# Optimization experiments

Measured on AMD Instinct MI355X. Metric: run time of the kernel, lower is better.

Reference implementation:

```python
import jax, jax.numpy as jnp
import numpy as np

FRS = np.array([1, 2, 4, 8, 16, 25, 36, 50, 75], dtype=np.float32)
N_EXPERTS = len(FRS)
N = 1048576
DIMS = [(4, 32), (32, 32), (32, 64), (64, 64)]


def setup_inputs() -> dict:
    key = jax.random.key(0)
    ks = jax.random.split(key, 2 + 8)
    # features: col 0 = framerate drawn from the known framerate set, cols 1:5 = affinity feats
    fr_idx = jax.random.randint(ks[0], (N,), 0, N_EXPERTS)
    framerates = jnp.asarray(FRS)[fr_idx]
    aff = jax.random.normal(ks[1], (N, 4), dtype=jnp.float32)
    features = jnp.concatenate([framerates[:, None], aff], axis=1)
    # stacked per-expert MLP params (torch Linear: y = x @ W.T + b; store W as [in,out])
    params = {}
    scale = 0.1
    for li, (din, dout) in enumerate(DIMS):
        params[f"W{li+1}"] = scale * jax.random.normal(ks[2 + 2 * li], (N_EXPERTS, din, dout), dtype=jnp.float32)
        params[f"b{li+1}"] = scale * jax.random.normal(ks[3 + 2 * li], (N_EXPERTS, dout), dtype=jnp.float32)
    return {"features": features, **params}


def _expert_mlp(x, W1, b1, W2, b2, W3, b3, W4, b4):
    h = jax.nn.relu(x @ W1 + b1)
    h = jax.nn.relu(h @ W2 + b2)
    h = jax.nn.relu(h @ W3 + b3)
    return h @ W4 + b4  # [N, 64]


def reference(features, W1, b1, W2, b2, W3, b3, W4, b4):
    frs = jnp.asarray(FRS)
    framerates = features[:, 0]
    x = features[:, 1:]  # [N, 4] (ignore_appr=False)
    # nearest-framerate expert index (argmin picks first min, matching find_index)
    k = jnp.argmin(jnp.abs(framerates[:, None] - frs[None, :]), axis=1)  # [N]
    pred = jnp.zeros(features.shape[0], dtype=features.dtype)
    for e in range(N_EXPERTS):  # fixed, small expert set
        out_e = _expert_mlp(x, W1[e], b1[e], W2[e], b2[e], W3[e], b3[e], W4[e], b4[e])
        pred = jnp.where(k == e, out_e.sum(axis=1), pred)
    return pred
```

## Files before the change

kernel.cpp:

```cpp
#include <hip/hip_runtime.h>
#include <stdint.h>

#define NEXP 9
#define FTHR 512
#define RPH 4
#define SBLK (FTHR * RPH)
#define PADSLK (SBLK + NEXP * 32)
#define MAXT 80
#define TBL_BYTES 7936
#define CLS_STRIDE 168

typedef float f32x4 __attribute__((ext_vector_type(4)));
typedef float f32x16 __attribute__((ext_vector_type(16)));
typedef _Float16 f16x8 __attribute__((ext_vector_type(8)));

struct alignas(16) I4 { int a, b, c, d; };
struct alignas(64) Q4 { f32x4 a, b, c, d; };

__device__ __forceinline__ int pk(float a, float b) {
    return __builtin_bit_cast(int, __builtin_amdgcn_cvt_pkrtz(a, b));
}
__device__ __forceinline__ f32x16 zero16() {
    f32x16 z;
#pragma unroll
    for (int r = 0; r < 16; ++r) z[r] = 0.f;
    return z;
}

__device__ __forceinline__ int expert_of(float fr) {
    const float frs[NEXP] = {1.f, 2.f, 4.f, 8.f, 16.f, 25.f, 36.f, 50.f, 75.f};
    int k = 0;
    float best = fabsf(fr - frs[0]);
#pragma unroll
    for (int e = 1; e < NEXP; ++e) {
        float d = fabsf(fr - frs[e]);
        if (d < best) { best = d; k = e; }
    }
    return k;
}

__global__ __launch_bounds__(256) void k_prep(const float* __restrict__ W1, const float* __restrict__ b1,
                                              const float* __restrict__ W2, const float* __restrict__ b2,
                                              const float* __restrict__ W3, const float* __restrict__ b3,
                                              const float* __restrict__ W4, const float* __restrict__ b4,
                                              char* __restrict__ tab) {
    int e = blockIdx.x;
    int tid = threadIdx.x;
    char* T = tab + (size_t)e * TBL_BYTES;

    __shared__ float psum[64][4];
    __shared__ float rs2[64];
    __shared__ float b4s_s;
    {
        int row = tid >> 2, q = tid & 3;
        const float* w = W4 + (size_t)e * 4096 + row * 64 + q * 16;
        f32x4 a = *(const f32x4*)(w + 0), b = *(const f32x4*)(w + 4);
        f32x4 c = *(const f32x4*)(w + 8), d = *(const f32x4*)(w + 12);
        psum[row][q] = (a.x + a.y + a.z + a.w) + (b.x + b.y + b.z + b.w)
                     + (c.x + c.y + c.z + c.w) + (d.x + d.y + d.z + d.w);
    }
    __syncthreads();
    if (tid < 64) {
        int l = tid, g = l >> 5, m = l & 31;
        rs2[l] = psum[l][0] + psum[l][1] + psum[l][2] + psum[l][3];
        float bp = b4[e * 64 + l];
#pragma unroll
        for (int d = 1; d < 64; d <<= 1) bp += __shfl_xor(bp, d, 64);
        if (l == 0) b4s_s = bp;

        {
            f16x8 v;
#pragma unroll
            for (int ei = 0; ei < 8; ++ei) {
                int k = g * 8 + ei;
                float w = (k < 4) ? W1[e * 128 + k * 32 + m] : (k == 4 ? b1[e * 32 + m] : 0.f);
                v[ei] = (_Float16)w;
            }
            *(f16x8*)(T + 0 * 1024 + l * 16) = v;
        }
#pragma unroll
        for (int kf = 0; kf < 2; ++kf) {
            f16x8 v;
#pragma unroll
            for (int ei = 0; ei < 8; ++ei) {
                int row = kf * 16 + (ei & 3) + 8 * (ei >> 2) + 4 * g;
                v[ei] = (_Float16)W2[e * 1024 + row * 32 + m];
            }
            *(f16x8*)(T + (1 + kf) * 1024 + l * 16) = v;
        }
#pragma unroll
        for (int t = 0; t < 2; ++t)
#pragma unroll
            for (int kf = 0; kf < 2; ++kf) {
                f16x8 v;
#pragma unroll
                for (int ei = 0; ei < 8; ++ei) {
                    int row = kf * 16 + (ei & 3) + 8 * (ei >> 2) + 4 * g;
                    v[ei] = (_Float16)W3[e * 2048 + row * 64 + t * 32 + m];
                }
                *(f16x8*)(T + (3 + t * 2 + kf) * 1024 + l * 16) = v;
            }
    }
    __syncthreads();
    if (tid < 32) {
        int g = tid >> 4, r = tid & 15;
        int row = (r & 3) + 8 * (r >> 2) + 4 * g;
        float* C = (float*)(T + 7168);
        C[0 * 32 + tid] = b2[e * 32 + row];
        C[1 * 32 + tid] = b3[e * 64 + row];
        C[2 * 32 + tid] = b3[e * 64 + 32 + row];
        C[3 * 32 + tid] = rs2[row];
        C[4 * 32 + tid] = rs2[32 + row];
        if (tid == 0) C[160] = b4s_s;
    }
}

__global__ __launch_bounds__(FTHR, 4) void k_main(const float* __restrict__ feat, int n,
                                                  const char* __restrict__ tab,
                                                  float* __restrict__ out) {
    __shared__ uint2 bx[PADSLK];
    __shared__ unsigned short bidx[PADSLK];
    __shared__ float cls[NEXP * CLS_STRIDE];
    __shared__ int lcnt[NEXP];
    __shared__ int pbase[NEXP];
    __shared__ int wbase[RPH][8][NEXP];
    __shared__ unsigned char tile_e[MAXT];
    __shared__ short tile_s[MAXT];
    __shared__ unsigned char tile_v[MAXT];
    __shared__ int nt_s;

    int bid = blockIdx.x, tid = threadIdx.x;
    int wid = tid >> 6, lane = tid & 63, g = lane >> 5, m = lane & 31;
    int gbase = bid * SBLK;

    if (tid < NEXP) lcnt[tid] = 0;
    {
        uint2 z = {0u, 0u};
#pragma unroll
        for (int q = 0; q < 5; ++q) {
            int o = q * FTHR + tid;
            if (o < PADSLK) bx[o] = z;
        }
    }
    {
        const float* tf = (const float*)tab;
        for (int idx = tid; idx < NEXP * 161; idx += FTHR) {
            int e = idx / 161, o = idx - e * 161;
            cls[e * CLS_STRIDE + o] = tf[e * (TBL_BYTES / 4) + 1792 + o];
        }
    }
    __syncthreads();

    int kk[RPH], rk[RPH];
    uint2 xw[RPH];
#pragma unroll
    for (int r = 0; r < RPH; ++r) {
        int i = gbase + r * FTHR + tid;
        int k = -1;
        uint2 w = {0u, 0u};
        if (i < n) {
            const float* f = feat + (size_t)i * 5;
            k = expert_of(f[0]);
            w.x = (unsigned)pk(f[1], f[2]);
            w.y = (unsigned)pk(f[3], f[4]);
        }
        kk[r] = k; xw[r] = w;
        unsigned long long myM = 0;
#pragma unroll
        for (int e = 0; e < NEXP; ++e) {
            unsigned long long mm = __ballot(k == e);
            if (k == e) myM = mm;
            if (lane == 0) {
                int c = __popcll(mm);
                wbase[r][wid][e] = c ? atomicAdd(&lcnt[e], c) : 0;
            }
        }
        rk[r] = __popcll(myM & ((1ull << lane) - 1ull));
    }
    __syncthreads();

    if (wid == 0) {
        int e = lane;
        int c = (e < NEXP) ? lcnt[e] : 0;
        int ntl = (c + 31) >> 5;
        int padc = ntl << 5;
        int sp = padc, st = ntl;
#pragma unroll
        for (int d = 1; d < 16; d <<= 1) {
            int a = __shfl_up(sp, d, 64);
            int b = __shfl_up(st, d, 64);
            if (lane >= d) { sp += a; st += b; }
        }
        if (e < NEXP) {
            int pb = sp - padc, tb = st - ntl;
            pbase[e] = pb;
            for (int j = 0; j < ntl; ++j) {
                tile_e[tb + j] = (unsigned char)e;
                tile_s[tb + j] = (short)(pb + j * 32);
                int v = c - j * 32;
                tile_v[tb + j] = (unsigned char)(v > 32 ? 32 : v);
            }
            if (e == NEXP - 1) nt_s = st;
        }
    }
    __syncthreads();

#pragma unroll
    for (int r = 0; r < RPH; ++r) {
        int k = kk[r];
        if (k >= 0) {
            int slot = pbase[k] + wbase[r][wid][k] + rk[r];
            bx[slot] = xw[r];
            bidx[slot] = (unsigned short)(r * FTHR + tid);
        }
    }
    __syncthreads();

    int nt = nt_s;
    int t0 = (wid * nt) >> 3, t1 = ((wid + 1) * nt) >> 3;
    int cur_e = -1;
    f16x8 A1 = {}, A2a = {}, A2b = {}, A30a = {}, A30b = {}, A31a = {}, A31b = {};
    f32x16 W40r = zero16(), W41r = zero16();
    float b4v = 0.f;
    const float* Cc = cls;
    for (int t = t0; t < t1; ++t) {
        int e = __builtin_amdgcn_readfirstlane((int)tile_e[t]);
        if (e != cur_e) {
            cur_e = e;
            const char* T = tab + (size_t)e * TBL_BYTES;
            A1 = *(const f16x8*)(T + 0 * 1024 + lane * 16);
            A2a = *(const f16x8*)(T + 1 * 1024 + lane * 16);
            A2b = *(const f16x8*)(T + 2 * 1024 + lane * 16);
            A30a = *(const f16x8*)(T + 3 * 1024 + lane * 16);
            A30b = *(const f16x8*)(T + 4 * 1024 + lane * 16);
            A31a = *(const f16x8*)(T + 5 * 1024 + lane * 16);
            A31b = *(const f16x8*)(T + 6 * 1024 + lane * 16);
            Cc = cls + e * CLS_STRIDE + g * 16;
            {
                Q4 q;
                const float* c = Cc + 3 * 32;
                q.a = *(const f32x4*)(c + 0); q.b = *(const f32x4*)(c + 4);
                q.c = *(const f32x4*)(c + 8); q.d = *(const f32x4*)(c + 12);
                W40r = __builtin_bit_cast(f32x16, q);
                const float* c2 = Cc + 4 * 32;
                q.a = *(const f32x4*)(c2 + 0); q.b = *(const f32x4*)(c2 + 4);
                q.c = *(const f32x4*)(c2 + 8); q.d = *(const f32x4*)(c2 + 12);
                W41r = __builtin_bit_cast(f32x16, q);
            }
            b4v = cls[e * CLS_STRIDE + 160];
        }
        auto ldC = [&](int mat) -> f32x16 {
            const float* c = Cc + mat * 32;
            Q4 q;
            q.a = *(const f32x4*)(c + 0);
            q.b = *(const f32x4*)(c + 4);
            q.c = *(const f32x4*)(c + 8);
            q.d = *(const f32x4*)(c + 12);
            return __builtin_bit_cast(f32x16, q);
        };

        int s = tile_s[t], v = tile_v[t];
        uint2 xv = bx[s + m];

        I4 b1i = {g ? 0 : (int)xv.x, g ? 0 : (int)xv.y, g ? 0 : 0x3C00, 0};
        f16x8 B1 = __builtin_bit_cast(f16x8, b1i);

        f32x16 d1 = __builtin_amdgcn_mfma_f32_32x32x16_f16(A1, B1, zero16(), 0, 0, 0);
#pragma unroll
        for (int r = 0; r < 16; ++r) d1[r] = fmaxf(d1[r], 0.f);
        I4 p0 = {pk(d1[0], d1[1]), pk(d1[2], d1[3]), pk(d1[4], d1[5]), pk(d1[6], d1[7])};
        I4 p1 = {pk(d1[8], d1[9]), pk(d1[10], d1[11]), pk(d1[12], d1[13]), pk(d1[14], d1[15])};
        f16x8 B2a = __builtin_bit_cast(f16x8, p0);
        f16x8 B2b = __builtin_bit_cast(f16x8, p1);

        f32x16 d2 = __builtin_amdgcn_mfma_f32_32x32x16_f16(A2a, B2a, ldC(0), 0, 0, 0);
        d2 = __builtin_amdgcn_mfma_f32_32x32x16_f16(A2b, B2b, d2, 0, 0, 0);
#pragma unroll
        for (int r = 0; r < 16; ++r) d2[r] = fmaxf(d2[r], 0.f);
        I4 q0 = {pk(d2[0], d2[1]), pk(d2[2], d2[3]), pk(d2[4], d2[5]), pk(d2[6], d2[7])};
        I4 q1 = {pk(d2[8], d2[9]), pk(d2[10], d2[11]), pk(d2[12], d2[13]), pk(d2[14], d2[15])};
        f16x8 B3a = __builtin_bit_cast(f16x8, q0);
        f16x8 B3b = __builtin_bit_cast(f16x8, q1);

        float acc = 0.f;
        {
            f32x16 d3 = __builtin_amdgcn_mfma_f32_32x32x16_f16(A30a, B3a, ldC(1), 0, 0, 0);
            d3 = __builtin_amdgcn_mfma_f32_32x32x16_f16(A30b, B3b, d3, 0, 0, 0);
#pragma unroll
            for (int r = 0; r < 16; ++r) acc += fmaxf(d3[r], 0.f) * W40r[r];
        }
        {
            f32x16 d3 = __builtin_amdgcn_mfma_f32_32x32x16_f16(A31a, B3a, ldC(2), 0, 0, 0);
            d3 = __builtin_amdgcn_mfma_f32_32x32x16_f16(A31b, B3b, d3, 0, 0, 0);
#pragma unroll
            for (int r = 0; r < 16; ++r) acc += fmaxf(d3[r], 0.f) * W41r[r];
        }
        acc += __shfl_xor(acc, 32, 64);
        float rres = acc + b4v;
        if (!g && m < v) out[gbase + (int)bidx[s + m]] = rres;
    }
}

__global__ __launch_bounds__(256) void k_fallback(const float* __restrict__ feat,
                                                  const float* __restrict__ W1, const float* __restrict__ b1,
                                                  const float* __restrict__ W2, const float* __restrict__ b2,
                                                  const float* __restrict__ W3, const float* __restrict__ b3,
                                                  const float* __restrict__ W4, const float* __restrict__ b4,
                                                  float* __restrict__ out, int n) {
    int i = blockIdx.x * 256 + threadIdx.x;
    if (i >= n) return;
    const float* f = feat + (size_t)i * 5;
    int e = expert_of(f[0]);
    float x0 = f[1], x1 = f[2], x2 = f[3], x3 = f[4];
    float h1[32], h2[32], h3[64];
    for (int j = 0; j < 32; ++j) {
        float a = b1[e * 32 + j];
        a += x0 * W1[e * 128 + 0 * 32 + j];
        a += x1 * W1[e * 128 + 1 * 32 + j];
        a += x2 * W1[e * 128 + 2 * 32 + j];
        a += x3 * W1[e * 128 + 3 * 32 + j];
        h1[j] = fmaxf(a, 0.f);
    }
    for (int j = 0; j < 32; ++j) h2[j] = b2[e * 32 + j];
    for (int i2 = 0; i2 < 32; ++i2)
        for (int j = 0; j < 32; ++j) h2[j] += h1[i2] * W2[e * 1024 + i2 * 32 + j];
    for (int j = 0; j < 32; ++j) h2[j] = fmaxf(h2[j], 0.f);
    for (int j = 0; j < 64; ++j) h3[j] = b3[e * 64 + j];
    for (int i2 = 0; i2 < 32; ++i2)
        for (int j = 0; j < 64; ++j) h3[j] += h2[i2] * W3[e * 2048 + i2 * 64 + j];
    float pred = 0.f;
    for (int o = 0; o < 64; ++o) pred += b4[e * 64 + o];
    for (int j = 0; j < 64; ++j) {
        float rsum = 0.f;
        for (int o = 0; o < 64; ++o) rsum += W4[e * 4096 + j * 64 + o];
        pred += fmaxf(h3[j], 0.f) * rsum;
    }
    out[i] = pred;
}

extern "C" void kernel_launch(void* const* d_in, const int* in_sizes, int n_in,
                              void* d_out, int out_size, void* d_ws, size_t ws_size,
                              hipStream_t stream) {
    const float* feat = (const float*)d_in[0];
    const float* W1 = (const float*)d_in[1];
    const float* b1 = (const float*)d_in[2];
    const float* W2 = (const float*)d_in[3];
    const float* b2 = (const float*)d_in[4];
    const float* W3 = (const float*)d_in[5];
    const float* b3 = (const float*)d_in[6];
    const float* W4 = (const float*)d_in[7];
    const float* b4 = (const float*)d_in[8];
    float* out = (float*)d_out;
    int n = in_sizes[0] / 5;

    const size_t need = (size_t)NEXP * TBL_BYTES;

    if (ws_size >= need) {
        char* tab = (char*)d_ws;
        k_prep<<<NEXP, 256, 0, stream>>>(W1, b1, W2, b2, W3, b3, W4, b4, tab);
        int nb = (n + SBLK - 1) / SBLK;
        k_main<<<nb, FTHR, 0, stream>>>(feat, n, tab, out);
    } else {
        k_fallback<<<(n + 255) / 256, 256, 0, stream>>>(feat, W1, b1, W2, b2, W3, b3, W4, b4, out, n);
    }
}
```

Measured before the change: 33.55 us.

## Move final layer reduction to MFMA, use packed f16 ReLU, halve rows per block

```diff
diff --git a/kernel.cpp b/kernel.cpp
--- a/kernel.cpp
+++ b/kernel.cpp
@@ -3,12 +3,12 @@
 
 #define NEXP 9
 #define FTHR 512
-#define RPH 4
+#define RPH 2
 #define SBLK (FTHR * RPH)
 #define PADSLK (SBLK + NEXP * 32)
-#define MAXT 80
+#define MAXT 48
 #define TBL_BYTES 7936
-#define CLS_STRIDE 168
+#define CLS_STRIDE 136
 
 typedef float f32x4 __attribute__((ext_vector_type(4)));
 typedef float f32x16 __attribute__((ext_vector_type(16)));
@@ -20,6 +20,13 @@
 __device__ __forceinline__ int pk(float a, float b) {
     return __builtin_bit_cast(int, __builtin_amdgcn_cvt_pkrtz(a, b));
 }
+__device__ __forceinline__ int pkh(float a, float b) {
+    int p = pk(a, b);
+    int r;
+    int z = 0;
+    asm("v_pk_max_f16 %0, %1, %2" : "=v"(r) : "v"(p), "v"(z));
+    return r;
+}
 __device__ __forceinline__ f32x16 zero16() {
     f32x16 z;
 #pragma unroll
@@ -28,15 +35,8 @@
 }
 
 __device__ __forceinline__ int expert_of(float fr) {
-    const float frs[NEXP] = {1.f, 2.f, 4.f, 8.f, 16.f, 25.f, 36.f, 50.f, 75.f};
-    int k = 0;
-    float best = fabsf(fr - frs[0]);
-#pragma unroll
-    for (int e = 1; e < NEXP; ++e) {
-        float d = fabsf(fr - frs[e]);
-        if (d < best) { best = d; k = e; }
-    }
-    return k;
+    return (fr > 1.5f) + (fr > 3.f) + (fr > 6.f) + (fr > 12.f)
+         + (fr > 20.5f) + (fr > 30.5f) + (fr > 43.f) + (fr > 62.5f);
 }
 
 __global__ __launch_bounds__(256) void k_prep(const float* __restrict__ W1, const float* __restrict__ b1,
@@ -109,18 +109,24 @@
         C[0 * 32 + tid] = b2[e * 32 + row];
         C[1 * 32 + tid] = b3[e * 64 + row];
         C[2 * 32 + tid] = b3[e * 64 + 32 + row];
-        C[3 * 32 + tid] = rs2[row];
-        C[4 * 32 + tid] = rs2[32 + row];
-        if (tid == 0) C[160] = b4s_s;
-    }
-}
-
-__global__ __launch_bounds__(FTHR, 4) void k_main(const float* __restrict__ feat, int n,
+        if (tid == 0) C[96] = b4s_s;
+        {
+            int f = tid >> 3, gg = (tid >> 2) & 1, j = tid & 3;
+            int t = f >> 1, h = f & 1;
+            int e0 = 2 * j, e1 = 2 * j + 1;
+            int r0 = t * 32 + h * 16 + (e0 & 3) + 8 * (e0 >> 2) + 4 * gg;
+            int r1 = t * 32 + h * 16 + (e1 & 3) + 8 * (e1 >> 2) + 4 * gg;
+            C[100 + tid] = __builtin_bit_cast(float, pk(rs2[r0], rs2[r1]));
+        }
+    }
+}
+
+__global__ __launch_bounds__(FTHR, 6) void k_main(const float* __restrict__ feat, int n,
                                                   const char* __restrict__ tab,
                                                   float* __restrict__ out) {
-    __shared__ uint2 bx[PADSLK];
+    __shared__ __align__(16) uint2 bx[PADSLK];
     __shared__ unsigned short bidx[PADSLK];
-    __shared__ float cls[NEXP * CLS_STRIDE];
+    __shared__ __align__(16) float cls[NEXP * CLS_STRIDE];
     __shared__ int lcnt[NEXP];
     __shared__ int pbase[NEXP];
     __shared__ int wbase[RPH][8][NEXP];
@@ -137,16 +143,16 @@
     {
         uint2 z = {0u, 0u};
 #pragma unroll
-        for (int q = 0; q < 5; ++q) {
+        for (int q = 0; q < 3; ++q) {
             int o = q * FTHR + tid;
             if (o < PADSLK) bx[o] = z;
         }
     }
     {
         const float* tf = (const float*)tab;
-        for (int idx = tid; idx < NEXP * 161; idx += FTHR) {
-            int e = idx / 161, o = idx - e * 161;
-            cls[e * CLS_STRIDE + o] = tf[e * (TBL_BYTES / 4) + 1792 + o];
+        for (int idx = tid; idx < NEXP * CLS_STRIDE; idx += FTHR) {
+            int e = idx / CLS_STRIDE, o = idx - e * CLS_STRIDE;
+            cls[idx] = tf[e * (TBL_BYTES / 4) + 1792 + o];
         }
     }
     __syncthreads();
@@ -220,9 +226,9 @@
     int t0 = (wid * nt) >> 3, t1 = ((wid + 1) * nt) >> 3;
     int cur_e = -1;
     f16x8 A1 = {}, A2a = {}, A2b = {}, A30a = {}, A30b = {}, A31a = {}, A31b = {};
-    f32x16 W40r = zero16(), W41r = zero16();
+    const float* Cc = cls;
+    const float* A4p = cls;
     float b4v = 0.f;
-    const float* Cc = cls;
     for (int t = t0; t < t1; ++t) {
         int e = __builtin_amdgcn_readfirstlane((int)tile_e[t]);
         if (e != cur_e) {
@@ -236,18 +242,8 @@
             A31a = *(const f16x8*)(T + 5 * 1024 + lane * 16);
             A31b = *(const f16x8*)(T + 6 * 1024 + lane * 16);
             Cc = cls + e * CLS_STRIDE + g * 16;
-            {
-                Q4 q;
-                const float* c = Cc + 3 * 32;
-                q.a = *(const f32x4*)(c + 0); q.b = *(const f32x4*)(c + 4);
-                q.c = *(const f32x4*)(c + 8); q.d = *(const f32x4*)(c + 12);
-                W40r = __builtin_bit_cast(f32x16, q);
-                const float* c2 = Cc + 4 * 32;
-                q.a = *(const f32x4*)(c2 + 0); q.b = *(const f32x4*)(c2 + 4);
-                q.c = *(const f32x4*)(c2 + 8); q.d = *(const f32x4*)(c2 + 12);
-                W41r = __builtin_bit_cast(f32x16, q);
-            }
-            b4v = cls[e * CLS_STRIDE + 160];
+            A4p = cls + e * CLS_STRIDE + 100 + g * 4;
+            b4v = cls[e * CLS_STRIDE + 96];
         }
         auto ldC = [&](int mat) -> f32x16 {
             const float* c = Cc + mat * 32;
@@ -258,6 +254,9 @@
             q.d = *(const f32x4*)(c + 12);
             return __builtin_bit_cast(f32x16, q);
         };
+        auto ldA4 = [&](int f) -> f16x8 {
+            return __builtin_bit_cast(f16x8, *(const f32x4*)(A4p + f * 8));
+        };
 
         int s = tile_s[t], v = tile_v[t];
         uint2 xv = bx[s + m];
@@ -266,38 +265,36 @@
         f16x8 B1 = __builtin_bit_cast(f16x8, b1i);
 
         f32x16 d1 = __builtin_amdgcn_mfma_f32_32x32x16_f16(A1, B1, zero16(), 0, 0, 0);
-#pragma unroll
-        for (int r = 0; r < 16; ++r) d1[r] = fmaxf(d1[r], 0.f);
-        I4 p0 = {pk(d1[0], d1[1]), pk(d1[2], d1[3]), pk(d1[4], d1[5]), pk(d1[6], d1[7])};
-        I4 p1 = {pk(d1[8], d1[9]), pk(d1[10], d1[11]), pk(d1[12], d1[13]), pk(d1[14], d1[15])};
+        I4 p0 = {pkh(d1[0], d1[1]), pkh(d1[2], d1[3]), pkh(d1[4], d1[5]), pkh(d1[6], d1[7])};
+        I4 p1 = {pkh(d1[8], d1[9]), pkh(d1[10], d1[11]), pkh(d1[12], d1[13]), pkh(d1[14], d1[15])};
         f16x8 B2a = __builtin_bit_cast(f16x8, p0);
         f16x8 B2b = __builtin_bit_cast(f16x8, p1);
 
         f32x16 d2 = __builtin_amdgcn_mfma_f32_32x32x16_f16(A2a, B2a, ldC(0), 0, 0, 0);
         d2 = __builtin_amdgcn_mfma_f32_32x32x16_f16(A2b, B2b, d2, 0, 0, 0);
-#pragma unroll
-        for (int r = 0; r < 16; ++r) d2[r] = fmaxf(d2[r], 0.f);
-        I4 q0 = {pk(d2[0], d2[1]), pk(d2[2], d2[3]), pk(d2[4], d2[5]), pk(d2[6], d2[7])};
-        I4 q1 = {pk(d2[8], d2[9]), pk(d2[10], d2[11]), pk(d2[12], d2[13]), pk(d2[14], d2[15])};
+        I4 q0 = {pkh(d2[0], d2[1]), pkh(d2[2], d2[3]), pkh(d2[4], d2[5]), pkh(d2[6], d2[7])};
+        I4 q1 = {pkh(d2[8], d2[9]), pkh(d2[10], d2[11]), pkh(d2[12], d2[13]), pkh(d2[14], d2[15])};
         f16x8 B3a = __builtin_bit_cast(f16x8, q0);
         f16x8 B3b = __builtin_bit_cast(f16x8, q1);
 
-        float acc = 0.f;
+        f32x16 d4;
         {
             f32x16 d3 = __builtin_amdgcn_mfma_f32_32x32x16_f16(A30a, B3a, ldC(1), 0, 0, 0);
             d3 = __builtin_amdgcn_mfma_f32_32x32x16_f16(A30b, B3b, d3, 0, 0, 0);
-#pragma unroll
-            for (int r = 0; r < 16; ++r) acc += fmaxf(d3[r], 0.f) * W40r[r];
+            I4 u0 = {pkh(d3[0], d3[1]), pkh(d3[2], d3[3]), pkh(d3[4], d3[5]), pkh(d3[6], d3[7])};
+            I4 u1 = {pkh(d3[8], d3[9]), pkh(d3[10], d3[11]), pkh(d3[12], d3[13]), pkh(d3[14], d3[15])};
+            d4 = __builtin_amdgcn_mfma_f32_32x32x16_f16(ldA4(0), __builtin_bit_cast(f16x8, u0), zero16(), 0, 0, 0);
+            d4 = __builtin_amdgcn_mfma_f32_32x32x16_f16(ldA4(1), __builtin_bit_cast(f16x8, u1), d4, 0, 0, 0);
         }
         {
             f32x16 d3 = __builtin_amdgcn_mfma_f32_32x32x16_f16(A31a, B3a, ldC(2), 0, 0, 0);
             d3 = __builtin_amdgcn_mfma_f32_32x32x16_f16(A31b, B3b, d3, 0, 0, 0);
-#pragma unroll
-            for (int r = 0; r < 16; ++r) acc += fmaxf(d3[r], 0.f) * W41r[r];
-        }
-        acc += __shfl_xor(acc, 32, 64);
-        float rres = acc + b4v;
-        if (!g && m < v) out[gbase + (int)bidx[s + m]] = rres;
+            I4 u0 = {pkh(d3[0], d3[1]), pkh(d3[2], d3[3]), pkh(d3[4], d3[5]), pkh(d3[6], d3[7])};
+            I4 u1 = {pkh(d3[8], d3[9]), pkh(d3[10], d3[11]), pkh(d3[12], d3[13]), pkh(d3[14], d3[15])};
+            d4 = __builtin_amdgcn_mfma_f32_32x32x16_f16(ldA4(2), __builtin_bit_cast(f16x8, u0), d4, 0, 0, 0);
+            d4 = __builtin_amdgcn_mfma_f32_32x32x16_f16(ldA4(3), __builtin_bit_cast(f16x8, u1), d4, 0, 0, 0);
+        }
+        if (!g && m < v) out[gbase + (int)bidx[s + m]] = d4[0] + b4v;
     }
 }
 
```

Result: no change. 33.93 us (+1.1%).
